# Performance work log

Hardware: AMD Instinct MI355X
Metric: run time of the kernel (lower is better)

## Reference

```python
import jax, jax.numpy as jnp
import numpy as np

KS = 3
STRIDE = 1
PAD = 1


def conv2d(x, w, b=None, stride=1, pad=0):
    out = jax.lax.conv_general_dilated(
        x, w, (stride, stride), [(pad, pad), (pad, pad)],
        dimension_numbers=('NCHW', 'OIHW', 'NCHW'))
    if b is not None:
        out = out + b[None, :, None, None]
    return out


def _get_p(offset, ks, stride):
    # offset: (b, 2N, h, w); returns sampling coords p = p_0 + p_n + offset
    b, c2, h, w = offset.shape
    N = c2 // 2
    r = (ks - 1) // 2
    pn_x, pn_y = jnp.meshgrid(jnp.arange(-r, r + 1), jnp.arange(-r, r + 1), indexing='ij')
    p_n = jnp.concatenate([pn_x.reshape(-1), pn_y.reshape(-1)]).astype(offset.dtype)  # (2N,)
    p0_x, p0_y = jnp.meshgrid(jnp.arange(1, h * stride + 1, stride),
                              jnp.arange(1, w * stride + 1, stride), indexing='ij')
    p0 = jnp.concatenate([jnp.broadcast_to(p0_x, (N, h, w)),
                          jnp.broadcast_to(p0_y, (N, h, w))], 0).astype(offset.dtype)  # (2N,h,w)
    return offset + p_n[None, :, None, None] + p0[None]


def _gather_hw(src, qx, qy):
    # src: (b,c,H,W); qx,qy: (b,h,w,N) int -> (b,c,h,w,N)
    b, c, H, W = src.shape
    flat = src.reshape(b, c, H * W)
    idx = (qx * W + qy).reshape(b, -1)
    out = jax.vmap(lambda f, i: f[:, i])(flat, idx)  # (b,c,h*w*N)
    return out.reshape(b, c, qx.shape[1], qx.shape[2], qx.shape[3])


def _bilinear(src_pad, p, Hc, Wc, N):
    # p: (b,h,w,2N); clamp bounds (Hc,Wc) follow the torch code (may differ from src_pad dims)
    px, py = p[..., :N], p[..., N:]
    fx, fy = jnp.floor(px), jnp.floor(py)
    qlt_x = jnp.clip(fx, 0, Hc - 1).astype(jnp.int32)
    qlt_y = jnp.clip(fy, 0, Wc - 1).astype(jnp.int32)
    qrb_x = jnp.clip(fx + 1, 0, Hc - 1).astype(jnp.int32)
    qrb_y = jnp.clip(fy + 1, 0, Wc - 1).astype(jnp.int32)
    pxc = jnp.clip(px, 0, Hc - 1)
    pyc = jnp.clip(py, 0, Wc - 1)
    g_lt = (1 + (qlt_x - pxc)) * (1 + (qlt_y - pyc))
    g_rb = (1 - (qrb_x - pxc)) * (1 - (qrb_y - pyc))
    g_lb = (1 + (qlt_x - pxc)) * (1 - (qrb_y - pyc))
    g_rt = (1 - (qrb_x - pxc)) * (1 + (qlt_y - pyc))
    v_lt = _gather_hw(src_pad, qlt_x, qlt_y)
    v_rb = _gather_hw(src_pad, qrb_x, qrb_y)
    v_lb = _gather_hw(src_pad, qlt_x, qrb_y)
    v_rt = _gather_hw(src_pad, qrb_x, qlt_y)
    return (g_lt[:, None] * v_lt + g_rb[:, None] * v_rb
            + g_lb[:, None] * v_lb + g_rt[:, None] * v_rt)


def setup_inputs() -> dict:
    key = jax.random.key(0)
    k1, k2, k3, k4 = jax.random.split(key, 4)
    B, C, H, W = 2, 64, 128, 128
    OUTC, KSZ = 64, KS
    N = KSZ * KSZ
    x = jax.random.normal(k1, (B, C, H, W), dtype=jnp.float32)
    depth = jax.random.uniform(k2, (B, 1, H, W), dtype=jnp.float32)
    w_p = jax.random.normal(k3, (2 * N, C, 3, 3), dtype=jnp.float32) * 0.01
    b_p = jnp.zeros((2 * N,), dtype=jnp.float32)
    w_conv = jax.random.normal(k4, (OUTC, C, KSZ, KSZ), dtype=jnp.float32) * 0.05
    return {'x': x, 'depth': depth, 'w_p': w_p, 'b_p': b_p, 'w_conv': w_conv}


def reference(x, depth, w_p, b_p, w_conv):
    ks, stride, pad = KS, STRIDE, PAD
    N = ks * ks
    b, c, H, W = x.shape
    offset = conv2d(x, w_p, b_p, stride=stride, pad=1)  # (b, 2N, h, w)
    depth_pad = jnp.pad(depth, ((0, 0), (0, 0), (pad, pad), (pad, pad)))
    # pass 1: sample depth; torch clamps against UNPADDED x dims here (quirk preserved)
    p = jnp.transpose(_get_p(offset, ks, stride), (0, 2, 3, 1))  # (b,h,w,2N)
    depth_offset = _bilinear(depth_pad, p, H, W, N)  # (b,1,h,w,N)
    depth_diff = jnp.abs(depth[..., None] - depth_offset)  # (b,1,h,w,N)
    depth_weight = jnp.exp(-4.0 * depth_diff) + 0.25
    dw = jnp.concatenate([depth_weight, depth_weight], axis=-1)  # (b,1,h,w,2N)
    dw = jnp.transpose(dw, (0, 4, 2, 3, 1))[..., 0]  # (b,2N,h,w)
    offset = offset * dw
    # pass 2: sample x from padded x, clamped to padded dims
    x_pad = jnp.pad(x, ((0, 0), (0, 0), (pad, pad), (pad, pad)))
    Hp, Wp = x_pad.shape[2], x_pad.shape[3]
    p = jnp.transpose(_get_p(offset, ks, stride), (0, 2, 3, 1))
    x_offset = _bilinear(x_pad, p, Hp, Wp, N)  # (b,c,h,w,N)
    m = jnp.exp(-1.0 * depth_diff)  # (b,1,h,w,N), broadcasts over c
    x_offset = x_offset * m
    # reshape (b,c,h,w,N) -> (b,c,h*ks,w*ks) matching _reshape_x_offset
    b2, c2, h, w, _ = x_offset.shape
    xo = x_offset.reshape(b2, c2, h, w, ks, ks)
    xo = jnp.transpose(xo, (0, 1, 2, 4, 3, 5)).reshape(b2, c2, h * ks, w * ks)
    out = conv2d(xo, w_conv, None, stride=ks, pad=0)  # (b,outc,h,w)
    return out
```

## Files before the change

kernel.cpp:

```cpp
#include <hip/hip_runtime.h>
#include <math.h>


typedef __attribute__((ext_vector_type(8))) short bf16x8;
typedef __attribute__((ext_vector_type(4))) short s16x4;
typedef __attribute__((ext_vector_type(4))) float f32x4;

#define MFMA16(a, b, c) __builtin_amdgcn_mfma_f32_16x16x32_bf16((a), (b), (c), 0, 0, 0)

__device__ __forceinline__ float bf2f(short v) {
    return __uint_as_float(((unsigned)(unsigned short)v) << 16);
}
__device__ __forceinline__ short f2bf(float f) {
    unsigned u = __float_as_uint(f);
    u = u + 0x7fffu + ((u >> 16) & 1u);
    return (short)(u >> 16);
}

__global__ __launch_bounds__(256) void k_prep(const float* __restrict__ x,
                                              const float* __restrict__ w_conv,
                                              const float* __restrict__ w_p,
                                              short* __restrict__ xT,
                                              short* __restrict__ xTlo,
                                              short* __restrict__ wK,
                                              short* __restrict__ wPh,
                                              short* __restrict__ wPl) {
    __shared__ short sH[128][72];
    __shared__ short sL[128][72];
    int bid = blockIdx.x;
    int tid = threadIdx.x;
    if (bid < 256) {
        int p = tid & 127;
        int halfc = tid >> 7;
        int pix0 = bid << 7;
        int b = pix0 >> 14;
        const float* xb = x + (size_t)b * 64 * 16384 + (pix0 & 16383);
#pragma unroll
        for (int cc = 0; cc < 8; ++cc) {
            int c0 = cc * 8 + halfc * 4;
            union { short s[4]; s16x4 v; } hi, lo;
#pragma unroll
            for (int e = 0; e < 4; ++e) {
                float v = xb[(c0 + e) * 16384 + p];
                short hb = f2bf(v);
                hi.s[e] = hb;
                lo.s[e] = f2bf(v - bf2f(hb));
            }
            *reinterpret_cast<s16x4*>(&sH[p][c0]) = hi.v;
            *reinterpret_cast<s16x4*>(&sL[p][c0]) = lo.v;
        }
        __syncthreads();
        short* xTo = xT   + ((size_t)pix0 << 6);
        short* xLo = xTlo + ((size_t)pix0 << 6);
#pragma unroll
        for (int r = 0; r < 4; ++r) {
            int u = (r << 8) + tid;
            int pp = u >> 3, ch8 = u & 7;
            *reinterpret_cast<bf16x8*>(xTo + pp * 64 + ch8 * 8) =
                *reinterpret_cast<const bf16x8*>(&sH[pp][ch8 * 8]);
            *reinterpret_cast<bf16x8*>(xLo + pp * 64 + ch8 * 8) =
                *reinterpret_cast<const bf16x8*>(&sL[pp][ch8 * 8]);
        }
    } else {
        int idx = (bid - 256) * 256 + tid;
        if (idx >= 55296) return;
        if (idx < 36864) {
            int e = idx & 7, o = (idx >> 3) & 63, h = (idx >> 9) & 3, s = idx >> 11;
            int k = s * 32 + h * 8 + e;
            int n = k >> 6, c = k & 63;
            wK[idx] = f2bf(w_conv[o * 576 + c * 9 + n]);
        } else {
            int j = idx - 36864;
            int e = j & 7, m = (j >> 3) & 31, h = (j >> 8) & 3, s = j >> 10;
            int k = s * 32 + h * 8 + e;
            int t = k >> 6, c = k & 63;
            float v = (m < 18) ? w_p[m * 576 + c * 9 + t] : 0.f;
            short hb = f2bf(v);
            wPh[j] = hb;
            wPl[j] = f2bf(v - bf2f(hb));
        }
    }
}

__global__ __launch_bounds__(512, 4) void k_fused(const short* __restrict__ xT,
                                                  const short* __restrict__ xTlo,
                                                  const short* __restrict__ wPh,
                                                  const short* __restrict__ wPl,
                                                  const short* __restrict__ wK,
                                                  const float* __restrict__ depth,
                                                  const float* __restrict__ b_p,
                                                  float* __restrict__ out) {
    __shared__ __align__(16) char smem[79360];
    short* win    = (short*)smem;
    float* dwin   = (float*)(smem + 44160);
    float* part1  = (float*)(smem + 45568);
    float* offs   = (float*)(smem + 55808);
    float* pmw    = (float*)(smem + 60928);
    float* accred = (float*)smem;
    float* obuf   = (float*)(smem + 16384);

    int tid = threadIdx.x;
    int lane = tid & 63;
    int wv = tid >> 6;
    int l15 = lane & 15, h = lane >> 4;
    int ps = wv & 3;
    int kh = wv >> 2;
    int p0 = ps << 4;
    int bid = blockIdx.x;
    int swz = (bid & 7) * 64 + (bid >> 3);
    int pb = swz << 6;
    int b = pb >> 14, i = (pb & 16383) >> 7, j0 = pb & 127;
    const short* xTb  = xT   + ((size_t)b << 20);
    const short* xTlb = xTlo + ((size_t)b << 20);
    const float* db = depth + (b << 14);

    for (int u = tid; u < 2760; u += 512) {
        int c8 = u & 7, px = u >> 3;
        int wr = px / 69, wc = px % 69;
        int r = i - 2 + wr, c = j0 - 2 + wc;
        bf16x8 v = {0, 0, 0, 0, 0, 0, 0, 0};
        if ((unsigned)r < 128u && (unsigned)c < 128u)
            v = *reinterpret_cast<const bf16x8*>(xTb + ((size_t)(r * 128 + c) << 6) + c8 * 8);
        *reinterpret_cast<bf16x8*>((char*)win + px * 128 + ((c8 ^ (px & 7)) << 4)) = v;
    }
    for (int u = tid; u < 345; u += 512) {
        int wr = u / 69, wc = u % 69;
        int r = i - 2 + wr, c = j0 - 2 + wc;
        dwin[u] = ((unsigned)r < 128u && (unsigned)c < 128u) ? db[r * 128 + c] : 0.f;
    }
    __syncthreads();

    f32x4 acc0 = {0.f, 0.f, 0.f, 0.f}, acc1 = {0.f, 0.f, 0.f, 0.f};
    int c8p = kh * 4 + h;
#pragma unroll
    for (int t = 0; t < 9; ++t) {
        int s_ = t * 2 + kh;
        int wp = (t / 3 + 1) * 69 + (p0 + l15 + t % 3 + 1);
        bf16x8 bh = *reinterpret_cast<const bf16x8*>(
            (char*)win + wp * 128 + ((c8p ^ (wp & 7)) << 4));
        int si = i + t / 3 - 1;
        int sj = j0 + p0 + l15 + t % 3 - 1;
        bf16x8 bl = {0, 0, 0, 0, 0, 0, 0, 0};
        if ((unsigned)si < 128u && (unsigned)sj < 128u)
            bl = *reinterpret_cast<const bf16x8*>(
                xTlb + ((size_t)(si * 128 + sj) << 6) + c8p * 8);
        const short* wh_ = wPh + (size_t)((s_ * 4 + h) * 32 + l15) * 8;
        const short* wl_ = wPl + (size_t)((s_ * 4 + h) * 32 + l15) * 8;
        bf16x8 ah0 = *reinterpret_cast<const bf16x8*>(wh_);
        bf16x8 ah1 = *reinterpret_cast<const bf16x8*>(wh_ + 128);
        bf16x8 al0 = *reinterpret_cast<const bf16x8*>(wl_);
        bf16x8 al1 = *reinterpret_cast<const bf16x8*>(wl_ + 128);
        acc0 = MFMA16(ah0, bh, acc0);
        acc1 = MFMA16(ah1, bh, acc1);
        acc0 = MFMA16(ah0, bl, acc0);
        acc1 = MFMA16(ah1, bl, acc1);
        acc0 = MFMA16(al0, bh, acc0);
        acc1 = MFMA16(al1, bh, acc1);
    }
    {
        float* pp = part1 + ((ps * 2 + kh) * 16 + l15) * 20;
#pragma unroll
        for (int r = 0; r < 4; ++r) {
            pp[h * 4 + r] = acc0[r];
            int o1 = 16 + h * 4 + r;
            if (o1 < 18) pp[o1] = acc1[r];
        }
    }
    __syncthreads();
    for (int u = tid; u < 1152; u += 512) {
        int p = u / 18, o = u % 18;
        int pps = p >> 4, pl = p & 15;
        offs[p * 20 + o] = part1[((pps * 2) * 16 + pl) * 20 + o] +
                           part1[((pps * 2 + 1) * 16 + pl) * 20 + o] + b_p[o];
    }
    __syncthreads();

    for (int u = tid; u < 576; u += 512) {
        int p = u / 9, n = u % 9;
        float offx = offs[p * 20 + n];
        float offy = offs[p * 20 + 9 + n];
        float gx = (float)(n / 3 - 1 + i + 1);
        float gy = (float)(n % 3 - 1 + j0 + p + 1);
        float dctr = dwin[2 * 69 + p + 2];
        float p1x = offx + gx, p1y = offy + gy;
        float fx = floorf(p1x), fy = floorf(p1y);
        float qltx = fminf(fmaxf(fx, 0.f), 127.f);
        float qlty = fminf(fmaxf(fy, 0.f), 127.f);
        float qrbx = fminf(fmaxf(fx + 1.f, 0.f), 127.f);
        float qrby = fminf(fmaxf(fy + 1.f, 0.f), 127.f);
        float pxc = fminf(fmaxf(p1x, 0.f), 127.f);
        float pyc = fminf(fmaxf(p1y, 0.f), 127.f);
        float glt = (1.f + (qltx - pxc)) * (1.f + (qlty - pyc));
        float grb = (1.f - (qrbx - pxc)) * (1.f - (qrby - pyc));
        float glb = (1.f + (qltx - pxc)) * (1.f - (qrby - pyc));
        float grt = (1.f - (qrbx - pxc)) * (1.f + (qlty - pyc));
        int ilx = (int)qltx, ily = (int)qlty, irx = (int)qrbx, iry = (int)qrby;
        auto dv = [&](int qx, int qy) -> float {
            if (qx < 1 || qx > 128 || qy < 1 || qy > 128) return 0.f;
            int r = qx - 1, c = qy - 1;
            int wr = r - (i - 2), wc = c - (j0 - 2);
            if ((unsigned)wr < 5u && (unsigned)wc < 69u) return dwin[wr * 69 + wc];
            return db[r * 128 + c];
        };
        float dof = glt * dv(ilx, ily) + grb * dv(irx, iry) + glb * dv(ilx, iry) + grt * dv(irx, ily);
        float dd = fabsf(dctr - dof);
        float dwn = expf(-4.f * dd) + 0.25f;
        float mn = expf(-dd);
        float px = offx * dwn + gx;
        float py = offy * dwn + gy;
        float fx2 = floorf(px), fy2 = floorf(py);
        float xltx = fminf(fmaxf(fx2, 0.f), 129.f);
        float xlty = fminf(fmaxf(fy2, 0.f), 129.f);
        float xrbx = fminf(fmaxf(fx2 + 1.f, 0.f), 129.f);
        float xrby = fminf(fmaxf(fy2 + 1.f, 0.f), 129.f);
        float xpxc = fminf(fmaxf(px, 0.f), 129.f);
        float xpyc = fminf(fmaxf(py, 0.f), 129.f);
        float wlt = (1.f + (xltx - xpxc)) * (1.f + (xlty - xpyc));
        float wrb = (1.f - (xrbx - xpxc)) * (1.f - (xrby - xpyc));
        float wlb = (1.f + (xltx - xpxc)) * (1.f - (xrby - xpyc));
        float wrt = (1.f - (xrbx - xpxc)) * (1.f + (xlty - xpyc));
        int jlx = (int)xltx, jly = (int)xlty, jrx = (int)xrbx, jry = (int)xrby;
        float* d = pmw + u * 8;
        int* di = (int*)(d + 4);
        auto mk = [&](int qx, int qy, float gw, int slot) {
            bool ok = (qx >= 1 && qx <= 128 && qy >= 1 && qy <= 128);
            d[slot] = ok ? gw * mn : 0.f;
            int idx = 0;
            if (ok) {
                int r = qx - 1, c = qy - 1;
                int wr = r - (i - 2), wc = c - (j0 - 2);
                idx = ((unsigned)wr < 5u && (unsigned)wc < 69u) ? (wr * 69 + wc)
                                                                : (-1 - (r * 128 + c));
            }
            di[slot] = idx;
        };
        mk(jlx, jly, wlt, 0);
        mk(jrx, jry, wrb, 1);
        mk(jlx, jry, wlb, 2);
        mk(jrx, jly, wrt, 3);
    }
    __syncthreads();

    f32x4 A0 = {0.f, 0.f, 0.f, 0.f}, A1 = {0.f, 0.f, 0.f, 0.f};
    f32x4 A2 = {0.f, 0.f, 0.f, 0.f}, A3 = {0.f, 0.f, 0.f, 0.f};
    for (int n = kh; n < 9; n += 2) {
        const float* ww = pmw + (size_t)((p0 + l15) * 9 + n) * 8;
        float4 w4 = *reinterpret_cast<const float4*>(ww);
        int4 i4 = *reinterpret_cast<const int4*>(ww + 4);
        const short* wk0 = wK + (size_t)((n * 8 + h) * 64 + l15) * 8;
        const short* wk1 = wk0 + 2048;
        bf16x8 a00 = *reinterpret_cast<const bf16x8*>(wk0);
        bf16x8 a01 = *reinterpret_cast<const bf16x8*>(wk0 + 128);
        bf16x8 a02 = *reinterpret_cast<const bf16x8*>(wk0 + 256);
        bf16x8 a03 = *reinterpret_cast<const bf16x8*>(wk0 + 384);
        bf16x8 a10 = *reinterpret_cast<const bf16x8*>(wk1);
        bf16x8 a11 = *reinterpret_cast<const bf16x8*>(wk1 + 128);
        bf16x8 a12 = *reinterpret_cast<const bf16x8*>(wk1 + 256);
        bf16x8 a13 = *reinterpret_cast<const bf16x8*>(wk1 + 384);
        const int* ip = &i4.x;
        const float* wp = &w4.x;
#pragma unroll
        for (int t = 0; t < 4; ++t) {
            int idx = ip[t];
            float w = wp[t];
            bf16x8 th0, th1;
            if (idx >= 0) {
                const char* base = (char*)win + idx * 128;
                th0 = *reinterpret_cast<const bf16x8*>(base + ((h ^ (idx & 7)) << 4));
                th1 = *reinterpret_cast<const bf16x8*>(base + (((4 + h) ^ (idx & 7)) << 4));
            } else {
                int gp = -1 - idx;
                const short* gb = xTb + ((size_t)gp << 6) + h * 8;
                th0 = *reinterpret_cast<const bf16x8*>(gb);
                th1 = *reinterpret_cast<const bf16x8*>(gb + 32);
            }
            f32x4 Z = {0.f, 0.f, 0.f, 0.f};
            f32x4 D0 = MFMA16(a00, th0, Z);
            f32x4 D1 = MFMA16(a01, th0, Z);
            f32x4 D2 = MFMA16(a02, th0, Z);
            f32x4 D3 = MFMA16(a03, th0, Z);
            D0 = MFMA16(a10, th1, D0);
            D1 = MFMA16(a11, th1, D1);
            D2 = MFMA16(a12, th1, D2);
            D3 = MFMA16(a13, th1, D3);
            A0 += w * D0;
            A1 += w * D1;
            A2 += w * D2;
            A3 += w * D3;
        }
    }
    __syncthreads();
    if (kh == 1) {
        float* ar = accred + (ps * 64 + lane) * 16;
        *reinterpret_cast<f32x4*>(ar)      = A0;
        *reinterpret_cast<f32x4*>(ar + 4)  = A1;
        *reinterpret_cast<f32x4*>(ar + 8)  = A2;
        *reinterpret_cast<f32x4*>(ar + 12) = A3;
    }
    __syncthreads();
    if (kh == 0) {
        const float* ar = accred + (ps * 64 + lane) * 16;
        int col = p0 + l15;
#pragma unroll
        for (int r = 0; r < 4; ++r) {
            obuf[(h * 4 + r) * 66 + col]      = A0[r] + ar[r];
            obuf[(16 + h * 4 + r) * 66 + col] = A1[r] + ar[4 + r];
            obuf[(32 + h * 4 + r) * 66 + col] = A2[r] + ar[8 + r];
            obuf[(48 + h * 4 + r) * 66 + col] = A3[r] + ar[12 + r];
        }
    }
    __syncthreads();
#pragma unroll
    for (int r = 0; r < 8; ++r) {
        int u = (r << 9) + tid;
        int o = u >> 6, p = u & 63;
        out[((size_t)(b * 64 + o) << 14) + (i << 7) + j0 + p] = obuf[o * 66 + p];
    }
}

extern "C" void kernel_launch(void* const* d_in, const int* in_sizes, int n_in,
                              void* d_out, int out_size, void* d_ws, size_t ws_size,
                              hipStream_t stream) {
    (void)in_sizes; (void)n_in; (void)out_size; (void)ws_size;
    const float* x      = (const float*)d_in[0];
    const float* depth  = (const float*)d_in[1];
    const float* w_p    = (const float*)d_in[2];
    const float* b_p    = (const float*)d_in[3];
    const float* w_conv = (const float*)d_in[4];
    float* out = (float*)d_out;

    char* wsb = (char*)d_ws;
    short* xT   = (short*)wsb;
    short* xTlo = (short*)(wsb + 4194304);
    short* wK   = (short*)(wsb + 8388608);
    short* wPh  = (short*)(wsb + 8462336);
    short* wPl  = (short*)(wsb + 8499200);

    hipLaunchKernelGGL(k_prep,  dim3(472), dim3(256), 0, stream,
                       x, w_conv, w_p, xT, xTlo, wK, wPh, wPl);
    hipLaunchKernelGGL(k_fused, dim3(512), dim3(512), 0, stream,
                       xT, xTlo, wPh, wPl, wK, depth, b_p, out);
}
```

Before: 37.39 us.

## Split sampling table into weight/index arrays, balance tap loop, write output directly

The per-tap weights and indices are stored in two separate LDS arrays with vector stores. The tap loop is fully unrolled, and the ninth tap is split between the two half-waves so both do equal work; previously one half did five taps and the other four. The final LDS staging buffer and its extra barrier are removed, and the kh==0 waves write results straight to global memory in 16-column segments. The reduction stride is padded to 20 floats to avoid bank conflicts. In exchange, global stores are less coalesced and only half the waves issue them.

```diff
diff --git a/kernel.cpp b/kernel.cpp
--- a/kernel.cpp
+++ b/kernel.cpp
@@ -95,9 +95,9 @@
     float* dwin   = (float*)(smem + 44160);
     float* part1  = (float*)(smem + 45568);
     float* offs   = (float*)(smem + 55808);
-    float* pmw    = (float*)(smem + 60928);
+    float* pw4    = (float*)(smem + 60928);
+    int*   pi4    = (int*)(smem + 70144);
     float* accred = (float*)smem;
-    float* obuf   = (float*)(smem + 16384);
 
     int tid = threadIdx.x;
     int lane = tid & 63;
@@ -220,11 +220,11 @@
         float wlb = (1.f + (xltx - xpxc)) * (1.f - (xrby - xpyc));
         float wrt = (1.f - (xrbx - xpxc)) * (1.f + (xlty - xpyc));
         int jlx = (int)xltx, jly = (int)xlty, jrx = (int)xrbx, jry = (int)xrby;
-        float* d = pmw + u * 8;
-        int* di = (int*)(d + 4);
+        float w4o[4];
+        int i4o[4];
         auto mk = [&](int qx, int qy, float gw, int slot) {
             bool ok = (qx >= 1 && qx <= 128 && qy >= 1 && qy <= 128);
-            d[slot] = ok ? gw * mn : 0.f;
+            w4o[slot] = ok ? gw * mn : 0.f;
             int idx = 0;
             if (ok) {
                 int r = qx - 1, c = qy - 1;
@@ -232,21 +232,54 @@
                 idx = ((unsigned)wr < 5u && (unsigned)wc < 69u) ? (wr * 69 + wc)
                                                                 : (-1 - (r * 128 + c));
             }
-            di[slot] = idx;
+            i4o[slot] = idx;
         };
         mk(jlx, jly, wlt, 0);
         mk(jrx, jry, wrb, 1);
         mk(jlx, jry, wlb, 2);
         mk(jrx, jly, wrt, 3);
+        *reinterpret_cast<float4*>(pw4 + u * 4) = make_float4(w4o[0], w4o[1], w4o[2], w4o[3]);
+        *reinterpret_cast<int4*>(pi4 + u * 4) = make_int4(i4o[0], i4o[1], i4o[2], i4o[3]);
     }
     __syncthreads();
 
     f32x4 A0 = {0.f, 0.f, 0.f, 0.f}, A1 = {0.f, 0.f, 0.f, 0.f};
     f32x4 A2 = {0.f, 0.f, 0.f, 0.f}, A3 = {0.f, 0.f, 0.f, 0.f};
-    for (int n = kh; n < 9; n += 2) {
-        const float* ww = pmw + (size_t)((p0 + l15) * 9 + n) * 8;
-        float4 w4 = *reinterpret_cast<const float4*>(ww);
-        int4 i4 = *reinterpret_cast<const int4*>(ww + 4);
+#define TAP_GEMM(IDX, W)                                                          \
+    {                                                                             \
+        int idx_ = (IDX);                                                         \
+        float w_ = (W);                                                           \
+        bf16x8 th0, th1;                                                          \
+        if (idx_ >= 0) {                                                          \
+            const char* base_ = (char*)win + idx_ * 128;                          \
+            th0 = *reinterpret_cast<const bf16x8*>(base_ + ((h ^ (idx_ & 7)) << 4));          \
+            th1 = *reinterpret_cast<const bf16x8*>(base_ + (((4 + h) ^ (idx_ & 7)) << 4));    \
+        } else {                                                                  \
+            int gp_ = -1 - idx_;                                                  \
+            const short* gb_ = xTb + ((size_t)gp_ << 6) + h * 8;                  \
+            th0 = *reinterpret_cast<const bf16x8*>(gb_);                          \
+            th1 = *reinterpret_cast<const bf16x8*>(gb_ + 32);                     \
+        }                                                                         \
+        f32x4 Z = {0.f, 0.f, 0.f, 0.f};                                           \
+        f32x4 D0 = MFMA16(a00, th0, Z);                                           \
+        f32x4 D1 = MFMA16(a01, th0, Z);                                           \
+        f32x4 D2 = MFMA16(a02, th0, Z);                                           \
+        f32x4 D3 = MFMA16(a03, th0, Z);                                           \
+        D0 = MFMA16(a10, th1, D0);                                                \
+        D1 = MFMA16(a11, th1, D1);                                                \
+        D2 = MFMA16(a12, th1, D2);                                                \
+        D3 = MFMA16(a13, th1, D3);                                                \
+        A0 += w_ * D0;                                                            \
+        A1 += w_ * D1;                                                            \
+        A2 += w_ * D2;                                                            \
+        A3 += w_ * D3;                                                            \
+    }
+#pragma unroll
+    for (int nn = 0; nn < 4; ++nn) {
+        int n = kh + nn * 2;
+        int uu = (p0 + l15) * 9 + n;
+        float4 w4 = *reinterpret_cast<const float4*>(pw4 + uu * 4);
+        int4 i4 = *reinterpret_cast<const int4*>(pi4 + uu * 4);
         const short* wk0 = wK + (size_t)((n * 8 + h) * 64 + l15) * 8;
         const short* wk1 = wk0 + 2048;
         bf16x8 a00 = *reinterpret_cast<const bf16x8*>(wk0);
@@ -257,41 +290,36 @@
         bf16x8 a11 = *reinterpret_cast<const bf16x8*>(wk1 + 128);
         bf16x8 a12 = *reinterpret_cast<const bf16x8*>(wk1 + 256);
         bf16x8 a13 = *reinterpret_cast<const bf16x8*>(wk1 + 384);
-        const int* ip = &i4.x;
-        const float* wp = &w4.x;
-#pragma unroll
-        for (int t = 0; t < 4; ++t) {
-            int idx = ip[t];
-            float w = wp[t];
-            bf16x8 th0, th1;
-            if (idx >= 0) {
-                const char* base = (char*)win + idx * 128;
-                th0 = *reinterpret_cast<const bf16x8*>(base + ((h ^ (idx & 7)) << 4));
-                th1 = *reinterpret_cast<const bf16x8*>(base + (((4 + h) ^ (idx & 7)) << 4));
-            } else {
-                int gp = -1 - idx;
-                const short* gb = xTb + ((size_t)gp << 6) + h * 8;
-                th0 = *reinterpret_cast<const bf16x8*>(gb);
-                th1 = *reinterpret_cast<const bf16x8*>(gb + 32);
-            }
-            f32x4 Z = {0.f, 0.f, 0.f, 0.f};
-            f32x4 D0 = MFMA16(a00, th0, Z);
-            f32x4 D1 = MFMA16(a01, th0, Z);
-            f32x4 D2 = MFMA16(a02, th0, Z);
-            f32x4 D3 = MFMA16(a03, th0, Z);
-            D0 = MFMA16(a10, th1, D0);
-            D1 = MFMA16(a11, th1, D1);
-            D2 = MFMA16(a12, th1, D2);
-            D3 = MFMA16(a13, th1, D3);
-            A0 += w * D0;
-            A1 += w * D1;
-            A2 += w * D2;
-            A3 += w * D3;
-        }
-    }
+        TAP_GEMM(i4.x, w4.x)
+        TAP_GEMM(i4.y, w4.y)
+        TAP_GEMM(i4.z, w4.z)
+        TAP_GEMM(i4.w, w4.w)
+    }
+    {
+        int uu = (p0 + l15) * 9 + 8;
+        float4 w4 = *reinterpret_cast<const float4*>(pw4 + uu * 4);
+        int4 i4 = *reinterpret_cast<const int4*>(pi4 + uu * 4);
+        const short* wk0 = wK + (size_t)((8 * 8 + h) * 64 + l15) * 8;
+        const short* wk1 = wk0 + 2048;
+        bf16x8 a00 = *reinterpret_cast<const bf16x8*>(wk0);
+        bf16x8 a01 = *reinterpret_cast<const bf16x8*>(wk0 + 128);
+        bf16x8 a02 = *reinterpret_cast<const bf16x8*>(wk0 + 256);
+        bf16x8 a03 = *reinterpret_cast<const bf16x8*>(wk0 + 384);
+        bf16x8 a10 = *reinterpret_cast<const bf16x8*>(wk1);
+        bf16x8 a11 = *reinterpret_cast<const bf16x8*>(wk1 + 128);
+        bf16x8 a12 = *reinterpret_cast<const bf16x8*>(wk1 + 256);
+        bf16x8 a13 = *reinterpret_cast<const bf16x8*>(wk1 + 384);
+        int idxA = kh ? i4.z : i4.x;
+        float wA  = kh ? w4.z : w4.x;
+        int idxB = kh ? i4.w : i4.y;
+        float wB  = kh ? w4.w : w4.y;
+        TAP_GEMM(idxA, wA)
+        TAP_GEMM(idxB, wB)
+    }
+#undef TAP_GEMM
     __syncthreads();
     if (kh == 1) {
-        float* ar = accred + (ps * 64 + lane) * 16;
+        float* ar = accred + (ps * 64 + lane) * 20;
         *reinterpret_cast<f32x4*>(ar)      = A0;
         *reinterpret_cast<f32x4*>(ar + 4)  = A1;
         *reinterpret_cast<f32x4*>(ar + 8)  = A2;
@@ -299,22 +327,16 @@
     }
     __syncthreads();
     if (kh == 0) {
-        const float* ar = accred + (ps * 64 + lane) * 16;
-        int col = p0 + l15;
+        const float* ar = accred + (ps * 64 + lane) * 20;
+        int col = j0 + p0 + l15;
+        size_t orow = ((size_t)b << 20) + ((size_t)i << 7) + col;
 #pragma unroll
         for (int r = 0; r < 4; ++r) {
-            obuf[(h * 4 + r) * 66 + col]      = A0[r] + ar[r];
-            obuf[(16 + h * 4 + r) * 66 + col] = A1[r] + ar[4 + r];
-            obuf[(32 + h * 4 + r) * 66 + col] = A2[r] + ar[8 + r];
-            obuf[(48 + h * 4 + r) * 66 + col] = A3[r] + ar[12 + r];
-        }
-    }
-    __syncthreads();
-#pragma unroll
-    for (int r = 0; r < 8; ++r) {
-        int u = (r << 9) + tid;
-        int o = u >> 6, p = u & 63;
-        out[((size_t)(b * 64 + o) << 14) + (i << 7) + j0 + p] = obuf[o * 66 + p];
+            out[orow + ((size_t)(h * 4 + r) << 14)]      = A0[r] + ar[r];
+            out[orow + ((size_t)(16 + h * 4 + r) << 14)] = A1[r] + ar[4 + r];
+            out[orow + ((size_t)(32 + h * 4 + r) << 14)] = A2[r] + ar[8 + r];
+            out[orow + ((size_t)(48 + h * 4 + r) << 14)] = A3[r] + ar[12 + r];
+        }
     }
 }
 
```

New measurement: 127.0 us. 240% more time.
